# Kernel tuning notes

Hardware: AMD Instinct MI355X
Metric: run time of the kernel (lower is better)

The kernel has to match this reference:

```python
import jax, jax.numpy as jnp
import numpy as np

NUM_GROUP = 4        # num_group: both chunk size of torch.split and number of groups used
TOP_CH = 27          # neighborhood_grid_width = 2*(max_displacement//stride2)+1 = 27
RADIUS = 13          # neighborhood_grid_radius * stride2
PAD_SHIFT = -10
MAX_ABS_SHIFT = RADIUS - PAD_SHIFT  # 23; shifts s = ch - 13 - 10 in [-23, 3]


def setup_inputs() -> dict:
    key = jax.random.key(0)
    k1, k2 = jax.random.split(key)
    N, C, H, W = 8, 16, 256, 512
    l_in = jax.random.normal(k1, (N, C, H, W), dtype=jnp.float32)
    r_in = jax.random.normal(k2, (N, C, H, W), dtype=jnp.float32)
    return {"l_in": l_in, "r_in": r_in}


def _corr_group(l_in, r_in):
    # l_in, r_in: [N, C, H, W]; only the first G*G = 16 channels are used
    # (torch.split(x, 4, dim=1) gives 4-channel chunks; forward consumes the first 4 chunks).
    N, C, H, W = l_in.shape
    G = NUM_GROUP
    f1 = l_in[:, : G * G].reshape(N, G, G, H, W)  # [N, group, ch_per_group, H, W]
    f2 = r_in[:, : G * G].reshape(N, G, G, H, W)
    P = MAX_ABS_SHIFT
    # Zero-pad width so out-of-range shifted positions contribute exactly 0,
    # matching the zeros left in `top` by the original slicing.
    f2p = jnp.pad(f2, ((0, 0), (0, 0), (0, 0), (0, 0), (P, P)))
    outs = []
    for ch in range(TOP_CH):  # fixed small loop over displacement channels
        s = ch - RADIUS + PAD_SHIFT  # s2o in [-23, 3]
        f2s = jax.lax.dynamic_slice_in_dim(f2p, P + s, W, axis=4)  # f2 shifted by s
        outs.append(jnp.einsum('ngchw,ngchw->nghw', f1, f2s))
    top = jnp.stack(outs, axis=2)  # [N, G, TOP_CH, H, W]
    sumelems = 1 * 1 * G  # kernel_size^2 * channels_per_group = 4
    return (top / sumelems).reshape(N, G * TOP_CH, H, W)


def reference(l_in, r_in):
    return _corr_group(l_in, r_in)  # [N, 108, H, W]
```

## Files before the change

### kernel.cpp

```cpp
#include <hip/hip_runtime.h>


#define TOP 27
#define GRP 4
#define CPG 4
#define HH 256
#define WW 512
#define NN 8
#define CIN 16

__global__ __launch_bounds__(256) void corr1d_kernel(
    const float* __restrict__ l, const float* __restrict__ r, float* __restrict__ out)
{
    const int t = threadIdx.x;
    int b = blockIdx.x;
    const int h = b & (HH - 1);
    b >>= 8;
    const int g = b & (GRP - 1);
    const int n = b >> 2;

    __shared__ __align__(16) float rsm[CPG][WW + 32];

    const size_t HWs = (size_t)HH * WW;
    const float* lbase = l + (((size_t)n * CIN + (size_t)g * CPG) * HH + h) * WW;
    const float* rbase = r + (((size_t)n * CIN + (size_t)g * CPG) * HH + h) * WW;

    float2 lv[CPG];
#pragma unroll
    for (int c = 0; c < CPG; ++c) {
        lv[c] = *(const float2*)(lbase + c * HWs + 2 * t);
        float2 rv = *(const float2*)(rbase + c * HWs + 2 * t);
        rsm[c][23 + 2 * t]     = rv.x;
        rsm[c][23 + 2 * t + 1] = rv.y;
    }
    if (t < 23) {
#pragma unroll
        for (int c = 0; c < CPG; ++c) rsm[c][t] = 0.0f;
    } else if (t >= 256 - 9) {
        const int i = t - (256 - 9);
#pragma unroll
        for (int c = 0; c < CPG; ++c) rsm[c][535 + i] = 0.0f;
    }
    __syncthreads();

    float acc0[TOP], acc1[TOP];
#pragma unroll
    for (int ch = 0; ch < TOP; ++ch) { acc0[ch] = 0.0f; acc1[ch] = 0.0f; }

#pragma unroll
    for (int c = 0; c < CPG; ++c) {
        float rv[28];
#pragma unroll
        for (int k = 0; k < 14; ++k) {
            float2 v = *(const float2*)&rsm[c][2 * t + 2 * k];
            rv[2 * k]     = v.x;
            rv[2 * k + 1] = v.y;
        }
        const float a0 = lv[c].x, a1 = lv[c].y;
#pragma unroll
        for (int ch = 0; ch < TOP; ++ch) {
            acc0[ch] += a0 * rv[ch];
            acc1[ch] += a1 * rv[ch + 1];
        }
    }

    float* obase = out + (((size_t)n * (GRP * TOP) + (size_t)g * TOP) * HH + h) * WW + 2 * t;
#pragma unroll
    for (int ch = 0; ch < TOP; ++ch) {
        float2 o;
        o.x = acc0[ch] * 0.25f;
        o.y = acc1[ch] * 0.25f;
        *(float2*)(obase + ch * HWs) = o;
    }
}

extern "C" void kernel_launch(void* const* d_in, const int* in_sizes, int n_in,
                              void* d_out, int out_size, void* d_ws, size_t ws_size,
                              hipStream_t stream) {
    const float* l = (const float*)d_in[0];
    const float* r = (const float*)d_in[1];
    float* out = (float*)d_out;
    dim3 grid(NN * GRP * HH);
    corr1d_kernel<<<grid, 256, 0, stream>>>(l, r, out);
}
```

Measured before the change: 110.3 us.

## Process four columns per thread, two rows per block, with nontemporal vector I/O

Each thread now computes four adjacent output columns instead of two, and each block covers two image rows, which halves the grid size. Shared-memory padding is realigned to 24 so the reads and writes can use 16-byte f32x4 accesses. Global loads and the output stores become nontemporal, which reduces cache pollution on this streaming kernel. Register pressure roughly doubles (108 accumulators per thread), which may lower occupancy.

```diff
diff --git a/kernel.cpp b/kernel.cpp
--- a/kernel.cpp
+++ b/kernel.cpp
@@ -8,69 +8,79 @@
 #define WW 512
 #define NN 8
 #define CIN 16
+#define PADL 24
+#define RROW (WW + 36)
+
+typedef float f32x4 __attribute__((ext_vector_type(4)));
 
 __global__ __launch_bounds__(256) void corr1d_kernel(
     const float* __restrict__ l, const float* __restrict__ r, float* __restrict__ out)
 {
-    const int t = threadIdx.x;
+    const int tid = threadIdx.x;
+    const int row = tid >> 7;
+    const int tw  = tid & 127;
+    const int w0  = tw << 2;
+
     int b = blockIdx.x;
-    const int h = b & (HH - 1);
-    b >>= 8;
+    const int hb = b & 127;
+    b >>= 7;
     const int g = b & (GRP - 1);
     const int n = b >> 2;
+    const int h = 2 * hb + row;
 
-    __shared__ __align__(16) float rsm[CPG][WW + 32];
+    __shared__ __align__(16) float rsm[2][CPG][RROW];
 
     const size_t HWs = (size_t)HH * WW;
     const float* lbase = l + (((size_t)n * CIN + (size_t)g * CPG) * HH + h) * WW;
     const float* rbase = r + (((size_t)n * CIN + (size_t)g * CPG) * HH + h) * WW;
 
-    float2 lv[CPG];
+    f32x4 lv[CPG];
 #pragma unroll
     for (int c = 0; c < CPG; ++c) {
-        lv[c] = *(const float2*)(lbase + c * HWs + 2 * t);
-        float2 rv = *(const float2*)(rbase + c * HWs + 2 * t);
-        rsm[c][23 + 2 * t]     = rv.x;
-        rsm[c][23 + 2 * t + 1] = rv.y;
+        lv[c] = __builtin_nontemporal_load((const f32x4*)(lbase + c * HWs + w0));
+        f32x4 rv4 = __builtin_nontemporal_load((const f32x4*)(rbase + c * HWs + w0));
+        *(f32x4*)&rsm[row][c][PADL + w0] = rv4;
     }
-    if (t < 23) {
+    if (tw < 24) {
 #pragma unroll
-        for (int c = 0; c < CPG; ++c) rsm[c][t] = 0.0f;
-    } else if (t >= 256 - 9) {
-        const int i = t - (256 - 9);
+        for (int c = 0; c < CPG; ++c) rsm[row][c][tw] = 0.0f;
+    } else if (tw >= 128 - 12) {
+        const int i = tw - 116;
 #pragma unroll
-        for (int c = 0; c < CPG; ++c) rsm[c][535 + i] = 0.0f;
+        for (int c = 0; c < CPG; ++c) rsm[row][c][536 + i] = 0.0f;
     }
     __syncthreads();
 
-    float acc0[TOP], acc1[TOP];
+    f32x4 acc[TOP];
 #pragma unroll
-    for (int ch = 0; ch < TOP; ++ch) { acc0[ch] = 0.0f; acc1[ch] = 0.0f; }
+    for (int ch = 0; ch < TOP; ++ch) acc[ch] = (f32x4)(0.0f);
 
 #pragma unroll
     for (int c = 0; c < CPG; ++c) {
-        float rv[28];
+        float rv[32];
 #pragma unroll
-        for (int k = 0; k < 14; ++k) {
-            float2 v = *(const float2*)&rsm[c][2 * t + 2 * k];
-            rv[2 * k]     = v.x;
-            rv[2 * k + 1] = v.y;
+        for (int k = 0; k < 8; ++k) {
+            f32x4 v = *(const f32x4*)&rsm[row][c][w0 + 4 * k];
+            rv[4 * k]     = v.x;
+            rv[4 * k + 1] = v.y;
+            rv[4 * k + 2] = v.z;
+            rv[4 * k + 3] = v.w;
         }
-        const float a0 = lv[c].x, a1 = lv[c].y;
+        const f32x4 a = lv[c];
 #pragma unroll
         for (int ch = 0; ch < TOP; ++ch) {
-            acc0[ch] += a0 * rv[ch];
-            acc1[ch] += a1 * rv[ch + 1];
+            acc[ch].x += a.x * rv[ch + 1];
+            acc[ch].y += a.y * rv[ch + 2];
+            acc[ch].z += a.z * rv[ch + 3];
+            acc[ch].w += a.w * rv[ch + 4];
         }
     }
 
-    float* obase = out + (((size_t)n * (GRP * TOP) + (size_t)g * TOP) * HH + h) * WW + 2 * t;
+    float* obase = out + (((size_t)n * (GRP * TOP) + (size_t)g * TOP) * HH + h) * WW + w0;
 #pragma unroll
     for (int ch = 0; ch < TOP; ++ch) {
-        float2 o;
-        o.x = acc0[ch] * 0.25f;
-        o.y = acc1[ch] * 0.25f;
-        *(float2*)(obase + ch * HWs) = o;
+        f32x4 o = acc[ch] * 0.25f;
+        __builtin_nontemporal_store(o, (f32x4*)(obase + ch * HWs));
     }
 }
 
@@ -80,6 +90,6 @@
     const float* l = (const float*)d_in[0];
     const float* r = (const float*)d_in[1];
     float* out = (float*)d_out;
-    dim3 grid(NN * GRP * HH);
+    dim3 grid(NN * GRP * (HH / 2));
     corr1d_kernel<<<grid, 256, 0, stream>>>(l, r, out);
 }
```

Result: no change. 111.5 us (+1.1%).

## Split displacement channels into three passes and use nontemporal loads/stores

Applied to the files above, without the earlier changes.

Splits the 27 displacement channels into three passes of 9, so each pass keeps only 18 accumulators and 12 shared-memory values in registers instead of 54 and 28, which should lower register pressure. The shared row padding becomes 24 so the shifted window reads and the right-row stores stay 8-byte aligned. Global loads and output stores switch to nontemporal builtins to avoid polluting the cache with streaming data. The cost is reading shared memory three times per channel.

```diff
diff --git a/kernel.cpp b/kernel.cpp
--- a/kernel.cpp
+++ b/kernel.cpp
@@ -8,69 +8,81 @@
 #define WW 512
 #define NN 8
 #define CIN 16
+#define PADL 24
+#define RROW (WW + 36)
+
+typedef float f32x2 __attribute__((ext_vector_type(2)));
 
 __global__ __launch_bounds__(256) void corr1d_kernel(
     const float* __restrict__ l, const float* __restrict__ r, float* __restrict__ out)
 {
     const int t = threadIdx.x;
+    const int w0 = 2 * t;
     int b = blockIdx.x;
     const int h = b & (HH - 1);
     b >>= 8;
     const int g = b & (GRP - 1);
     const int n = b >> 2;
 
-    __shared__ __align__(16) float rsm[CPG][WW + 32];
+    __shared__ __align__(16) float rsm[CPG][RROW];
 
     const size_t HWs = (size_t)HH * WW;
     const float* lbase = l + (((size_t)n * CIN + (size_t)g * CPG) * HH + h) * WW;
     const float* rbase = r + (((size_t)n * CIN + (size_t)g * CPG) * HH + h) * WW;
 
-    float2 lv[CPG];
+    f32x2 lv[CPG];
 #pragma unroll
     for (int c = 0; c < CPG; ++c) {
-        lv[c] = *(const float2*)(lbase + c * HWs + 2 * t);
-        float2 rv = *(const float2*)(rbase + c * HWs + 2 * t);
-        rsm[c][23 + 2 * t]     = rv.x;
-        rsm[c][23 + 2 * t + 1] = rv.y;
+        lv[c] = __builtin_nontemporal_load((const f32x2*)(lbase + c * HWs + w0));
+        f32x2 rv2 = __builtin_nontemporal_load((const f32x2*)(rbase + c * HWs + w0));
+        *(f32x2*)&rsm[c][PADL + w0] = rv2;
     }
-    if (t < 23) {
+    if (t < 24) {
 #pragma unroll
         for (int c = 0; c < CPG; ++c) rsm[c][t] = 0.0f;
-    } else if (t >= 256 - 9) {
-        const int i = t - (256 - 9);
+    } else if (t >= 256 - 12) {
+        const int i = t - 244;
 #pragma unroll
-        for (int c = 0; c < CPG; ++c) rsm[c][535 + i] = 0.0f;
+        for (int c = 0; c < CPG; ++c) rsm[c][536 + i] = 0.0f;
     }
     __syncthreads();
 
-    float acc0[TOP], acc1[TOP];
-#pragma unroll
-    for (int ch = 0; ch < TOP; ++ch) { acc0[ch] = 0.0f; acc1[ch] = 0.0f; }
+    float* obase = out + (((size_t)n * (GRP * TOP) + (size_t)g * TOP) * HH + h) * WW + w0;
+
+    const int c0s[3]  = {0, 9, 18};
+    const int offs[3] = {0, 10, 18};
+    const int ibs[3]  = {1, 0, 1};
 
 #pragma unroll
-    for (int c = 0; c < CPG; ++c) {
-        float rv[28];
+    for (int kk = 0; kk < 3; ++kk) {
+        const int c0 = c0s[kk], off = offs[kk], ib = ibs[kk];
+        float acc0[9], acc1[9];
 #pragma unroll
-        for (int k = 0; k < 14; ++k) {
-            float2 v = *(const float2*)&rsm[c][2 * t + 2 * k];
-            rv[2 * k]     = v.x;
-            rv[2 * k + 1] = v.y;
+        for (int ch = 0; ch < 9; ++ch) { acc0[ch] = 0.0f; acc1[ch] = 0.0f; }
+
+#pragma unroll
+        for (int c = 0; c < CPG; ++c) {
+            float rv[12];
+#pragma unroll
+            for (int k = 0; k < 6; ++k) {
+                f32x2 v = *(const f32x2*)&rsm[c][w0 + off + 2 * k];
+                rv[2 * k]     = v.x;
+                rv[2 * k + 1] = v.y;
+            }
+            const float a0 = lv[c].x, a1 = lv[c].y;
+#pragma unroll
+            for (int ch = 0; ch < 9; ++ch) {
+                acc0[ch] += a0 * rv[ib + ch];
+                acc1[ch] += a1 * rv[ib + ch + 1];
+            }
         }
-        const float a0 = lv[c].x, a1 = lv[c].y;
 #pragma unroll
-        for (int ch = 0; ch < TOP; ++ch) {
-            acc0[ch] += a0 * rv[ch];
-            acc1[ch] += a1 * rv[ch + 1];
+        for (int ch = 0; ch < 9; ++ch) {
+            f32x2 o;
+            o.x = acc0[ch] * 0.25f;
+            o.y = acc1[ch] * 0.25f;
+            __builtin_nontemporal_store(o, (f32x2*)(obase + (size_t)(c0 + ch) * HWs));
         }
-    }
-
-    float* obase = out + (((size_t)n * (GRP * TOP) + (size_t)g * TOP) * HH + h) * WW + 2 * t;
-#pragma unroll
-    for (int ch = 0; ch < TOP; ++ch) {
-        float2 o;
-        o.x = acc0[ch] * 0.25f;
-        o.y = acc1[ch] * 0.25f;
-        *(float2*)(obase + ch * HWs) = o;
     }
 }
 
```

After: 105.9 us, median of 2. -4.0%, faster.
